# Optimization experiments

Measured on AMD Instinct MI355X. Metric: run time of the kernel, lower is better.

## Reference

```python
import jax, jax.numpy as jnp
import numpy as np

N = 200000
NNZ = 6400000
E = 500000
IN_P, IN_F, IN_N = 62, 37, 37
HID, LAT, DEC_HID = 256, 128, 64


def _p(key, shape, scale=0.05):
    return scale * jax.random.normal(key, shape, dtype=jnp.float32)


def setup_inputs() -> dict:
    key = jax.random.key(0)
    ks = jax.random.split(key, 32)
    inp = {
        'x_process': jax.random.normal(ks[0], (N, IN_P), dtype=jnp.float32),
        'x_file': jax.random.normal(ks[1], (N, IN_F), dtype=jnp.float32),
        'x_network': jax.random.normal(ks[2], (N, IN_N), dtype=jnp.float32),
        'adj_rows': jax.random.randint(ks[3], (NNZ,), 0, N, dtype=jnp.int32),
        'adj_cols': jax.random.randint(ks[4], (NNZ,), 0, N, dtype=jnp.int32),
        'adj_vals': jax.random.uniform(ks[5], (NNZ,), dtype=jnp.float32) / 32.0,
        'edge_src': jax.random.randint(ks[6], (E,), 0, N, dtype=jnp.int32),
        'edge_dst': jax.random.randint(ks[7], (E,), 0, N, dtype=jnp.int32),
        # per-view encoder params (weights stored [in, out])
        'Wp1': _p(ks[8], (IN_P, HID)), 'bp1': jnp.zeros((HID,), jnp.float32),
        'Wp2': _p(ks[9], (HID, LAT)), 'bp2': jnp.zeros((LAT,), jnp.float32),
        'Wf1': _p(ks[10], (IN_F, HID)), 'bf1': jnp.zeros((HID,), jnp.float32),
        'Wf2': _p(ks[11], (HID, LAT)), 'bf2': jnp.zeros((LAT,), jnp.float32),
        'Wn1': _p(ks[12], (IN_N, HID)), 'bn1': jnp.zeros((HID,), jnp.float32),
        'Wn2': _p(ks[13], (HID, LAT)), 'bn2': jnp.zeros((LAT,), jnp.float32),
        # gates
        'Wgp': _p(ks[14], (LAT, 1)), 'bgp': jnp.zeros((1,), jnp.float32),
        'Wgf': _p(ks[15], (LAT, 1)), 'bgf': jnp.zeros((1,), jnp.float32),
        'Wgn': _p(ks[16], (LAT, 1)), 'bgn': jnp.zeros((1,), jnp.float32),
        # mlp edge decoder
        'Wd1': _p(ks[17], (4 * LAT, DEC_HID)), 'bd1': jnp.zeros((DEC_HID,), jnp.float32),
        'Wd2': _p(ks[18], (DEC_HID, 1)), 'bd2': jnp.zeros((1,), jnp.float32),
    }
    return inp


def _spmm(rows, cols, vals, x):
    # sparse (COO) adjacency @ dense x : gather cols, scale, scatter-add into rows
    return jax.ops.segment_sum(vals[:, None] * x[cols], rows, num_segments=N)


def _encode_view(x, rows, cols, vals, W1, b1, W2, b2):
    h = jax.nn.relu(_spmm(rows, cols, vals, x) @ W1 + b1)  # dropout=0 / eval mode
    return _spmm(rows, cols, vals, h) @ W2 + b2


def reference(x_process, x_file, x_network, adj_rows, adj_cols, adj_vals,
              edge_src, edge_dst,
              Wp1, bp1, Wp2, bp2, Wf1, bf1, Wf2, bf2, Wn1, bn1, Wn2, bn2,
              Wgp, bgp, Wgf, bgf, Wgn, bgn, Wd1, bd1, Wd2, bd2):
    zp = _encode_view(x_process, adj_rows, adj_cols, adj_vals, Wp1, bp1, Wp2, bp2)
    zf = _encode_view(x_file, adj_rows, adj_cols, adj_vals, Wf1, bf1, Wf2, bf2)
    zn = _encode_view(x_network, adj_rows, adj_cols, adj_vals, Wn1, bn1, Wn2, bn2)
    # multi-view softmax gating -> fused latent [N, LAT]
    scores = jnp.concatenate([zp @ Wgp + bgp, zf @ Wgf + bgf, zn @ Wgn + bgn], axis=1)
    alpha = jax.nn.softmax(scores, axis=1)
    z = alpha[:, 0:1] * zp + alpha[:, 1:2] * zf + alpha[:, 2:3] * zn
    # mlp edge decoder: gather src/dst, concat features, small MLP
    zs, zd = z[edge_src], z[edge_dst]
    feats = jnp.concatenate([zs, zd, zs * zd, jnp.abs(zs - zd)], axis=1)  # [E, 4*LAT]
    logits = jax.nn.relu(feats @ Wd1 + bd1) @ Wd2 + bd2
    return logits[:, 0]
```

## Files before the change

### kernel.cpp

```cpp
#include <hip/hip_runtime.h>
#include <math.h>

#define Nn 200000
#define NNZV 6400000
#define NE 500000
#define HID 256
#define LAT 128

typedef _Float16 h2 __attribute__((ext_vector_type(2)));
typedef _Float16 f16x4 __attribute__((ext_vector_type(4)));
typedef _Float16 f16x8 __attribute__((ext_vector_type(8)));
typedef float f32x4 __attribute__((ext_vector_type(4)));
typedef short s16x8 __attribute__((ext_vector_type(8)));
struct alignas(8) H4 { _Float16 h[4]; };

__device__ __forceinline__ float rdlanef(float v, int k){
  return __uint_as_float(__builtin_amdgcn_readlane(__float_as_uint(v), k));
}

__global__ __launch_bounds__(256) void k_zero(int* __restrict__ cnt){
  int i = blockIdx.x*256 + threadIdx.x;
  if(i < Nn) cnt[i] = 0;
}

__global__ __launch_bounds__(256) void k_count(const int* __restrict__ rows, int* __restrict__ cnt){
  int i = blockIdx.x*256 + threadIdx.x;
  if(i < NNZV) atomicAdd(&cnt[rows[i]], 1);
}

__global__ __launch_bounds__(512) void k_scan_block(const int* __restrict__ cnt, int* __restrict__ incl, int* __restrict__ bsum){
  __shared__ int s[512];
  int t = threadIdx.x;
  int i = blockIdx.x*512 + t;
  int v = (i < Nn) ? cnt[i] : 0;
  s[t] = v; __syncthreads();
  for(int off = 1; off < 512; off <<= 1){
    int x = (t >= off) ? s[t-off] : 0;
    __syncthreads();
    s[t] += x;
    __syncthreads();
  }
  if(i < Nn) incl[i] = s[t];
  if(t == 511) bsum[blockIdx.x] = s[t];
}

__global__ __launch_bounds__(512) void k_scan_bsum(int* __restrict__ bsum, int nb){
  __shared__ int s[512];
  int t = threadIdx.x;
  int v = (t < nb) ? bsum[t] : 0;
  s[t] = v; __syncthreads();
  for(int off = 1; off < 512; off <<= 1){
    int x = (t >= off) ? s[t-off] : 0;
    __syncthreads();
    s[t] += x;
    __syncthreads();
  }
  if(t < nb) bsum[t] = s[t] - v;
}

__global__ __launch_bounds__(256) void k_finish(const int* __restrict__ incl, const int* __restrict__ boff, int* __restrict__ row_ptr){
  int i = blockIdx.x*256 + threadIdx.x;
  if(i < Nn) row_ptr[i+1] = incl[i] + boff[i >> 9];
  if(i == 0) row_ptr[0] = 0;
}

__global__ __launch_bounds__(256) void k_initcur(const int* __restrict__ row_ptr, int* __restrict__ cur){
  int i = blockIdx.x*256 + threadIdx.x;
  if(i < Nn) cur[i] = row_ptr[i];
}

__global__ __launch_bounds__(256) void k_scatter(const int* __restrict__ rows, const int* __restrict__ cols,
    const float* __restrict__ vals, int* __restrict__ cur,
    int* __restrict__ cols_s, _Float16* __restrict__ vals_s){
  int i = blockIdx.x*256 + threadIdx.x;
  if(i >= NNZV) return;
  int r = rows[i];
  int j = atomicAdd(&cur[r], 1);
  cols_s[j] = cols[i];
  vals_s[j] = (_Float16)vals[i];
}

__global__ __launch_bounds__(256) void k_xpack(const float* __restrict__ xp, const float* __restrict__ xf,
    const float* __restrict__ xn, _Float16* __restrict__ xc0, _Float16* __restrict__ xtl){
  int idx = blockIdx.x*256 + threadIdx.x;
  int row = idx/18, c8 = idx - row*18;
  if(row >= Nn) return;
  H4 ha, hb;
  #pragma unroll
  for(int q = 0; q < 8; q++){
    int c = c8*8 + q;
    float x;
    if(c < 62)       x = xp[row*62 + c];
    else if(c < 99)  x = xf[row*37 + (c-62)];
    else if(c == 99) x = 0.f;
    else if(c < 137) x = xn[row*37 + (c-100)];
    else             x = 0.f;
    if(q < 4) ha.h[q] = (_Float16)x; else hb.h[q-4] = (_Float16)x;
  }
  if(c8 < 16){
    *(H4*)&xc0[(size_t)row*128 + c8*8]     = ha;
    *(H4*)&xc0[(size_t)row*128 + c8*8 + 4] = hb;
  } else {
    int t = (c8-16)*8;
    *(H4*)&xtl[(size_t)row*16 + t]     = ha;
    *(H4*)&xtl[(size_t)row*16 + t + 4] = hb;
  }
}

__global__ __launch_bounds__(256) void k_wpackF(
    const float* __restrict__ Wp1, const float* __restrict__ Wf1, const float* __restrict__ Wn1,
    const float* __restrict__ Wp2, const float* __restrict__ Wf2, const float* __restrict__ Wn2,
    _Float16* __restrict__ w1fp, _Float16* __restrict__ w1ff, _Float16* __restrict__ w1fn,
    _Float16* __restrict__ w2fp, _Float16* __restrict__ w2ff, _Float16* __restrict__ w2fn){
  int i = blockIdx.x*256 + threadIdx.x;
  if(i >= 18432) return;
  int v = i / 6144, rem = i - v*6144;
  const float* W1 = (v==0)?Wp1:((v==1)?Wf1:Wn1);
  const float* W2 = (v==0)?Wp2:((v==1)?Wf2:Wn2);
  _Float16* d1 = (v==0)?w1fp:((v==1)?w1ff:w1fn);
  _Float16* d2 = (v==0)?w2fp:((v==1)?w2ff:w2fn);
  int Kv = (v==0)?62:37;
  f16x8 o;
  if(rem < 2048){
    int kt = rem >> 10, r2 = rem & 1023;
    int nt = r2 >> 6, l = r2 & 63;
    int krow = kt*32 + (l>>4)*8, col = nt*16 + (l&15);
    #pragma unroll
    for(int j = 0; j < 8; j++){
      int k = krow + j;
      o[j] = (k < Kv) ? (_Float16)W1[k*256 + col] : (_Float16)0.f;
    }
    *(f16x8*)&d1[rem*8] = o;
  } else {
    int r = rem - 2048;
    int kt = r >> 9, nt = (r >> 6) & 7, l = r & 63;
    int krow = kt*32 + (l>>4)*8, col = nt*16 + (l&15);
    #pragma unroll
    for(int j = 0; j < 8; j++)
      o[j] = (_Float16)W2[(krow + j)*128 + col];
    *(f16x8*)&d2[r*8] = o;
  }
}

__global__ void k_wg2(const float* __restrict__ Wp2, const float* __restrict__ Wgp,
                      const float* __restrict__ Wf2, const float* __restrict__ Wgf,
                      const float* __restrict__ Wn2, const float* __restrict__ Wgn,
                      float* __restrict__ wg2){
  int k = threadIdx.x;
  float p = 0.f, f = 0.f, n = 0.f;
  for(int c = 0; c < 128; c++){
    p = fmaf(Wp2[k*128 + c], Wgp[c], p);
    f = fmaf(Wf2[k*128 + c], Wgf[c], f);
    n = fmaf(Wn2[k*128 + c], Wgn[c], n);
  }
  wg2[k] = p; wg2[256 + k] = f; wg2[512 + k] = n;
}

__global__ void k_const(const float* b2p, const float* Wgp, const float* bgp,
                        const float* b2f, const float* Wgf, const float* bgf,
                        const float* b2n, const float* Wgn, const float* bgn,
                        float* c3){
  int l = threadIdx.x;
  float p = 0.f, f = 0.f, n = 0.f;
  for(int j = l; j < LAT; j += 64){
    p += b2p[j]*Wgp[j];
    f += b2f[j]*Wgf[j];
    n += b2n[j]*Wgn[j];
  }
  #pragma unroll
  for(int off = 32; off >= 1; off >>= 1){
    p += __shfl_xor(p, off);
    f += __shfl_xor(f, off);
    n += __shfl_xor(n, off);
  }
  if(l == 0){ c3[0] = p + bgp[0]; c3[1] = f + bgf[0]; c3[2] = n + bgn[0]; }
}

__device__ __forceinline__ void encode_view(
    int tid, int row0, int voff, int Kv, int vidx,
    const _Float16 (*sT)[152], _Float16 (*sTv)[72], _Float16 (*hT)[264],
    const _Float16* __restrict__ w1frag, const float* __restrict__ b1,
    const _Float16* __restrict__ w2frag, const float* __restrict__ wg2v,
    _Float16* __restrict__ Y3, float* __restrict__ yg4f){
  int w = tid >> 6, l = tid & 63;
  int kg = l >> 4, er = l & 15;
  int mrow = (w & 1)*16 + er;

  {
    int row = tid >> 3, c0 = (tid & 7)*8;
    f16x8 vv;
    #pragma unroll
    for(int q = 0; q < 8; q++){
      int c = c0 + q;
      vv[q] = (c < Kv) ? sT[row][voff + c] : (_Float16)0.f;
    }
    *(f16x8*)&sTv[row][c0] = vv;
  }
  __syncthreads();

  {
    f16x8 a0 = *(const f16x8*)&sTv[mrow][kg*8];
    f16x8 a1 = *(const f16x8*)&sTv[mrow][32 + kg*8];
    int ntb = (w >> 1)*8;
    #pragma unroll
    for(int nt8 = 0; nt8 < 8; nt8++){
      int nt = ntb + nt8;
      f16x8 b0 = *(const f16x8*)&w1frag[(size_t)((0*16 + nt)*64 + l)*8];
      f16x8 b1v = *(const f16x8*)&w1frag[(size_t)((1*16 + nt)*64 + l)*8];
      f32x4 acc = {0.f, 0.f, 0.f, 0.f};
      acc = __builtin_amdgcn_mfma_f32_16x16x32_f16(a0, b0, acc, 0, 0, 0);
      acc = __builtin_amdgcn_mfma_f32_16x16x32_f16(a1, b1v, acc, 0, 0, 0);
      int col = nt*16 + er;
      float bb = b1[col];
      #pragma unroll
      for(int j = 0; j < 4; j++)
        hT[(w & 1)*16 + kg*4 + j][col] = (_Float16)fmaxf(acc[j] + bb, 0.f);
    }
  }
  __syncthreads();

  {
    int row = tid >> 3, cg = tid & 7;
    float p = 0.f;
    #pragma unroll 8
    for(int kk = 0; kk < 32; kk++)
      p = fmaf((float)hT[row][cg*32 + kk], wg2v[cg*32 + kk], p);
    p += __shfl_xor(p, 1);
    p += __shfl_xor(p, 2);
    p += __shfl_xor(p, 4);
    if((tid & 7) == 0) yg4f[(size_t)(row0 + row)*4 + vidx] = p;
  }

  {
    f16x8 af[8];
    #pragma unroll
    for(int kt = 0; kt < 8; kt++)
      af[kt] = *(const f16x8*)&hT[mrow][kt*32 + kg*8];
    __syncthreads();
    _Float16* yst = &hT[0][0];
    int ntb = (w >> 1)*4;
    #pragma unroll
    for(int nt4 = 0; nt4 < 4; nt4++){
      int nt = ntb + nt4;
      f32x4 acc = {0.f, 0.f, 0.f, 0.f};
      #pragma unroll
      for(int kt = 0; kt < 8; kt++){
        f16x8 bf = *(const f16x8*)&w2frag[(size_t)((kt*8 + nt)*64 + l)*8];
        acc = __builtin_amdgcn_mfma_f32_16x16x32_f16(af[kt], bf, acc, 0, 0, 0);
      }
      int col = nt*16 + er;
      #pragma unroll
      for(int j = 0; j < 4; j++)
        yst[((w & 1)*16 + kg*4 + j)*132 + col] = (_Float16)acc[j];
    }
    __syncthreads();
    int row = tid >> 3, c0 = (tid & 7)*16;
    f16x8 y0 = *(const f16x8*)&yst[row*132 + c0];
    f16x8 y1 = *(const f16x8*)&yst[row*132 + c0 + 8];
    _Float16* yo = &Y3[(size_t)(row0 + row)*384 + vidx*128 + c0];
    *(f16x8*)yo       = y0;
    *(f16x8*)(yo + 8) = y1;
  }
  __syncthreads();
}

__global__ __launch_bounds__(256, 5) void k_encfused(
    const int* __restrict__ row_ptr, const int* __restrict__ cols_s, const _Float16* __restrict__ vals_s,
    const _Float16* __restrict__ xc0, const _Float16* __restrict__ xtl,
    const _Float16* __restrict__ w1fp, const float* __restrict__ bp1, const _Float16* __restrict__ w2fp,
    const _Float16* __restrict__ w1ff, const float* __restrict__ bf1, const _Float16* __restrict__ w2ff,
    const _Float16* __restrict__ w1fn, const float* __restrict__ bn1, const _Float16* __restrict__ w2fn,
    const float* __restrict__ wg2,
    _Float16* __restrict__ Y3, float* __restrict__ yg4f){
  __shared__ _Float16 sT[32][152];
  __shared__ _Float16 sTv[32][72];
  __shared__ _Float16 hT[32][264];
  int tid = threadIdx.x;
  int lane = tid & 63, wid = tid >> 6;
  int hl = lane & 31;
  int half = lane >> 5;
  int base = lane & 32;
  int row0 = blockIdx.x * 32;
  bool hast = (hl < 4);
  const char* xc0b = (const char*)xc0;
  const char* xtlb = (const char*)xtl;

  for(int p = 0; p < 4; p++){
    int rr = wid*8 + p*2 + half;
    int r = row0 + rr;
    int start = row_ptr[r], end = row_ptr[r+1];
    int len = end - start;
    int lenO = __shfl(len, lane ^ 32);
    int lenmax = len > lenO ? len : lenO;
    float a0 = 0.f, a1 = 0.f, a2 = 0.f, a3 = 0.f;
    float t0 = 0.f, t1 = 0.f, t2 = 0.f, t3 = 0.f;
    for(int j0 = 0; j0 < lenmax; j0 += 32){
      int m = len - j0; if(m > 32) m = 32; if(m < 0) m = 0;
      int mO = lenO - j0; if(mO > 32) mO = 32; if(mO < 0) mO = 0;
      int mmax = m > mO ? m : mO;
      int mycol = 0; float myval = 0.f;
      if(hl < m){
        mycol = cols_s[start + j0 + hl];
        myval = (float)vals_s[start + j0 + hl];
      }
      int mpad = (mmax + 3) & ~3;
      for(int k = 0; k < mpad; k += 4){
        #pragma unroll
        for(int q = 0; q < 4; q++){
          int c = __shfl(mycol, base + k + q);
          float v = __shfl(myval, base + k + q);
          f16x4 xa = *(const f16x4*)(xc0b + (((unsigned)c) << 8) + hl*8);
          a0 = fmaf((float)xa[0], v, a0);
          a1 = fmaf((float)xa[1], v, a1);
          a2 = fmaf((float)xa[2], v, a2);
          a3 = fmaf((float)xa[3], v, a3);
          if(hast){
            f16x4 xb = *(const f16x4*)(xtlb + ((unsigned)c)*32u + hl*8);
            t0 = fmaf((float)xb[0], v, t0);
            t1 = fmaf((float)xb[1], v, t1);
            t2 = fmaf((float)xb[2], v, t2);
            t3 = fmaf((float)xb[3], v, t3);
          }
        }
      }
    }
    h2 s01; s01[0] = (_Float16)a0; s01[1] = (_Float16)a1;
    h2 s23; s23[0] = (_Float16)a2; s23[1] = (_Float16)a3;
    *(h2*)&sT[rr][4*hl]     = s01;
    *(h2*)&sT[rr][4*hl + 2] = s23;
    if(hast){
      h2 u01; u01[0] = (_Float16)t0; u01[1] = (_Float16)t1;
      h2 u23; u23[0] = (_Float16)t2; u23[1] = (_Float16)t3;
      *(h2*)&sT[rr][128 + 4*hl]     = u01;
      *(h2*)&sT[rr][128 + 4*hl + 2] = u23;
    }
  }
  __syncthreads();

  encode_view(tid, row0, 0,   62, 0, sT, sTv, hT, w1fp, bp1, w2fp, wg2,       Y3, yg4f);
  encode_view(tid, row0, 62,  37, 1, sT, sTv, hT, w1ff, bf1, w2ff, wg2 + 256, Y3, yg4f);
  encode_view(tid, row0, 100, 37, 2, sT, sTv, hT, w1fn, bn1, w2fn, wg2 + 512, Y3, yg4f);
}

__global__ __launch_bounds__(256, 8) void k_spmm2f(
    const int* __restrict__ row_ptr, const int* __restrict__ cols_s, const _Float16* __restrict__ vals_s,
    const _Float16* __restrict__ Y3,
    const float4* __restrict__ yg4, const float* __restrict__ c3,
    const float* __restrict__ b2p, const float* __restrict__ b2f, const float* __restrict__ b2n,
    _Float16* __restrict__ z){
  int tid = threadIdx.x;
  int lane = tid & 63;
  int r = blockIdx.x*4 + (tid >> 6);
  int start = row_ptr[r], end = row_ptr[r+1];
  unsigned lo = lane*4;
  float ap0=0.f, ap1=0.f, af0=0.f, af1=0.f, an0=0.f, an1=0.f;
  float scp=0.f, scf=0.f, scn=0.f;
  const char* Yb = (const char*)Y3;
  for(int j0 = start; j0 < end; j0 += 64){
    int m = end - j0; if(m > 64) m = 64;
    int mycol = 0; float myval = 0.f;
    if(lane < m){
      mycol = cols_s[j0 + lane];
      myval = (float)vals_s[j0 + lane];
      float4 g = yg4[mycol];
      scp = fmaf(myval, g.x, scp);
      scf = fmaf(myval, g.y, scf);
      scn = fmaf(myval, g.z, scn);
    }
    int mpad = (m + 3) & ~3;
    for(int k = 0; k < mpad; k += 4){
      #pragma unroll
      for(int q = 0; q < 4; q++){
        int c = __builtin_amdgcn_readlane(mycol, k + q);
        float v = rdlanef(myval, k + q);
        const char* p = Yb + ((unsigned)c)*768u + lo;
        h2 yp = *(const h2*)(p);
        h2 yf = *(const h2*)(p + 256);
        h2 yn = *(const h2*)(p + 512);
        ap0 = fmaf((float)yp[0], v, ap0); ap1 = fmaf((float)yp[1], v, ap1);
        af0 = fmaf((float)yf[0], v, af0); af1 = fmaf((float)yf[1], v, af1);
        an0 = fmaf((float)yn[0], v, an0); an1 = fmaf((float)yn[1], v, an1);
      }
    }
  }
  #pragma unroll
  for(int off = 32; off >= 1; off >>= 1){
    scp += __shfl_xor(scp, off);
    scf += __shfl_xor(scf, off);
    scn += __shfl_xor(scn, off);
  }
  float sp = scp + c3[0], sf = scf + c3[1], sn = scn + c3[2];
  float mx = fmaxf(sp, fmaxf(sf, sn));
  float ep = expf(sp - mx), ef = expf(sf - mx), en = expf(sn - mx);
  float inv = 1.f / (ep + ef + en);
  float A0 = ep*inv, A1 = ef*inv, A2 = en*inv;
  int o = lane*2;
  float2 bp = *(const float2*)&b2p[o];
  float2 bf = *(const float2*)&b2f[o];
  float2 bn = *(const float2*)&b2n[o];
  float z0 = A0*(ap0 + bp.x) + A1*(af0 + bf.x) + A2*(an0 + bn.x);
  float z1 = A0*(ap1 + bp.y) + A1*(af1 + bf.y) + A2*(an1 + bn.y);
  h2 uz; uz[0] = (_Float16)z0; uz[1] = (_Float16)z1;
  *(h2*)&z[(size_t)r*LAT + o] = uz;
}

#define DEC_TILES (NE/16)
__global__ __launch_bounds__(256) void k_dec(
    const _Float16* __restrict__ z, const int* __restrict__ esrc, const int* __restrict__ edst,
    const float* __restrict__ Wd1, const float* __restrict__ bd1,
    const float* __restrict__ Wd2, const float* __restrict__ bd2, float* __restrict__ out){
  __shared__ float part[4][16][68];
  int tid = threadIdx.x;
  int w  = tid >> 6;
  int l  = tid & 63;
  int erow = l & 15;
  int kg   = l >> 4;

  f16x8 bfr[4][4];
  #pragma unroll
  for(int kt = 0; kt < 4; kt++){
    #pragma unroll
    for(int nt = 0; nt < 4; nt++){
      f16x8 bb;
      #pragma unroll
      for(int j = 0; j < 8; j++)
        bb[j] = (_Float16)Wd1[(w*128 + kt*32 + kg*8 + j)*64 + nt*16 + erow];
      bfr[kt][nt] = bb;
    }
  }

  int n0 = (tid & 15) * 4;
  int e2 = tid >> 4;
  float4 bb1 = *(const float4*)&bd1[n0];
  float4 w2v = *(const float4*)&Wd2[n0];
  float bias2 = bd2[0];

  for(int tile = blockIdx.x; tile < DEC_TILES; tile += gridDim.x){
    int e = tile*16 + erow;
    int si = esrc[e], di = edst[e];
    const f16x8* zs = (const f16x8*)&z[(size_t)si*LAT];
    const f16x8* zd = (const f16x8*)&z[(size_t)di*LAT];
    f16x8 afr[4];
    if(w == 0){
      #pragma unroll
      for(int kt = 0; kt < 4; kt++) afr[kt] = zs[kt*4 + kg];
    } else if(w == 1){
      #pragma unroll
      for(int kt = 0; kt < 4; kt++) afr[kt] = zd[kt*4 + kg];
    } else if(w == 2){
      #pragma unroll
      for(int kt = 0; kt < 4; kt++) afr[kt] = zs[kt*4 + kg] * zd[kt*4 + kg];
    } else {
      #pragma unroll
      for(int kt = 0; kt < 4; kt++){
        f16x8 d = zs[kt*4 + kg] - zd[kt*4 + kg];
        s16x8 m = __builtin_bit_cast(s16x8, d) & (short)0x7fff;
        afr[kt] = __builtin_bit_cast(f16x8, m);
      }
    }
    f32x4 zero = {0.f, 0.f, 0.f, 0.f};
    f32x4 acc[4] = {zero, zero, zero, zero};
    #pragma unroll
    for(int kt = 0; kt < 4; kt++){
      #pragma unroll
      for(int nt = 0; nt < 4; nt++)
        acc[nt] = __builtin_amdgcn_mfma_f32_16x16x32_f16(afr[kt], bfr[kt][nt], acc[nt], 0, 0, 0);
    }
    #pragma unroll
    for(int nt = 0; nt < 4; nt++){
      #pragma unroll
      for(int j = 0; j < 4; j++)
        part[w][kg*4 + j][nt*16 + erow] = acc[nt][j];
    }
    __syncthreads();
    float s0 = part[0][e2][n0+0] + part[1][e2][n0+0] + part[2][e2][n0+0] + part[3][e2][n0+0];
    float s1 = part[0][e2][n0+1] + part[1][e2][n0+1] + part[2][e2][n0+1] + part[3][e2][n0+1];
    float s2 = part[0][e2][n0+2] + part[1][e2][n0+2] + part[2][e2][n0+2] + part[3][e2][n0+2];
    float s3 = part[0][e2][n0+3] + part[1][e2][n0+3] + part[2][e2][n0+3] + part[3][e2][n0+3];
    float p = fmaxf(s0 + bb1.x, 0.f)*w2v.x + fmaxf(s1 + bb1.y, 0.f)*w2v.y
            + fmaxf(s2 + bb1.z, 0.f)*w2v.z + fmaxf(s3 + bb1.w, 0.f)*w2v.w;
    #pragma unroll
    for(int off = 1; off < 16; off <<= 1) p += __shfl_xor(p, off);
    if((tid & 15) == 0) out[tile*16 + e2] = p + bias2;
    __syncthreads();
  }
}

extern "C" void kernel_launch(void* const* d_in, const int* in_sizes, int n_in,
                              void* d_out, int out_size, void* d_ws, size_t ws_size,
                              hipStream_t stream) {
  const float* xp  = (const float*)d_in[0];
  const float* xf  = (const float*)d_in[1];
  const float* xn  = (const float*)d_in[2];
  const int* arows = (const int*)d_in[3];
  const int* acols = (const int*)d_in[4];
  const float* avals = (const float*)d_in[5];
  const int* esrc  = (const int*)d_in[6];
  const int* edst  = (const int*)d_in[7];
  const float* Wp1 = (const float*)d_in[8];  const float* bp1 = (const float*)d_in[9];
  const float* Wp2 = (const float*)d_in[10]; const float* bp2 = (const float*)d_in[11];
  const float* Wf1 = (const float*)d_in[12]; const float* bf1 = (const float*)d_in[13];
  const float* Wf2 = (const float*)d_in[14]; const float* bf2w = (const float*)d_in[15];
  const float* Wn1 = (const float*)d_in[16]; const float* bn1 = (const float*)d_in[17];
  const float* Wn2 = (const float*)d_in[18]; const float* bn2 = (const float*)d_in[19];
  const float* Wgp = (const float*)d_in[20]; const float* bgp = (const float*)d_in[21];
  const float* Wgf = (const float*)d_in[22]; const float* bgf = (const float*)d_in[23];
  const float* Wgn = (const float*)d_in[24]; const float* bgn = (const float*)d_in[25];
  const float* Wd1 = (const float*)d_in[26]; const float* bd1 = (const float*)d_in[27];
  const float* Wd2 = (const float*)d_in[28]; const float* bd2 = (const float*)d_in[29];
  float* out = (float*)d_out;
  (void)in_sizes; (void)n_in; (void)out_size; (void)ws_size;

  char* base = (char*)d_ws;
  size_t off = 0;
  auto alloc = [&](size_t nbytes) -> char* {
    off = (off + 255) & ~(size_t)255;
    char* p = base + off;
    off += nbytes;
    return p;
  };
  int*      row_ptr = (int*)     alloc((size_t)(Nn + 1) * 4);
  int*      cols_s  = (int*)     alloc((size_t)NNZV * 4);
  _Float16* vals_s  = (_Float16*)alloc((size_t)NNZV * 2);
  _Float16* xcat0   = (_Float16*)alloc((size_t)Nn * 128 * 2);
  _Float16* xtail   = (_Float16*)alloc((size_t)Nn * 16 * 2);
  _Float16* Y3      = (_Float16*)alloc((size_t)Nn * 384 * 2);
  float*    yg4     = (float*)   alloc((size_t)Nn * 4 * 4);
  float*    c3      = (float*)   alloc(256);
  float*    wg2     = (float*)   alloc(3 * 256 * 4);
  _Float16* w1fp = (_Float16*)alloc(16384*2);
  _Float16* w1ff = (_Float16*)alloc(16384*2);
  _Float16* w1fn = (_Float16*)alloc(16384*2);
  _Float16* w2fp = (_Float16*)alloc(32768*2);
  _Float16* w2ff = (_Float16*)alloc(32768*2);
  _Float16* w2fn = (_Float16*)alloc(32768*2);
  _Float16* z = xcat0;
  int* cur  = (int*)((char*)xcat0);
  int* incl = (int*)((char*)xcat0 + 1000000);
  int* bsum = (int*)((char*)xcat0 + 2000000);

  int NB = (Nn + 511) / 512;

  k_zero   <<<(Nn + 255)/256, 256, 0, stream>>>(cur);
  k_count  <<<(NNZV + 255)/256, 256, 0, stream>>>(arows, cur);
  k_scan_block<<<NB, 512, 0, stream>>>(cur, incl, bsum);
  k_scan_bsum<<<1, 512, 0, stream>>>(bsum, NB);
  k_finish <<<(Nn + 255)/256, 256, 0, stream>>>(incl, bsum, row_ptr);
  k_initcur<<<(Nn + 255)/256, 256, 0, stream>>>(row_ptr, cur);
  k_scatter<<<(NNZV + 255)/256, 256, 0, stream>>>(arows, acols, avals, cur, cols_s, vals_s);

  k_xpack<<<(Nn*18 + 255)/256, 256, 0, stream>>>(xp, xf, xn, xcat0, xtail);
  k_wpackF<<<72, 256, 0, stream>>>(Wp1, Wf1, Wn1, Wp2, Wf2, Wn2,
                                   w1fp, w1ff, w1fn, w2fp, w2ff, w2fn);
  k_wg2<<<1, 256, 0, stream>>>(Wp2, Wgp, Wf2, Wgf, Wn2, Wgn, wg2);
  k_const<<<1, 64, 0, stream>>>(bp2, Wgp, bgp, bf2w, Wgf, bgf, bn2, Wgn, bgn, c3);

  k_encfused<<<Nn/32, 256, 0, stream>>>(row_ptr, cols_s, vals_s, xcat0, xtail,
      w1fp, bp1, w2fp,  w1ff, bf1, w2ff,  w1fn, bn1, w2fn,  wg2,
      Y3, yg4);

  k_spmm2f<<<Nn/4, 256, 0, stream>>>(row_ptr, cols_s, vals_s, Y3,
      (const float4*)yg4, c3, bp2, bf2w, bn2, z);

  k_dec<<<2048, 256, 0, stream>>>(z, esrc, edst, Wd1, bd1, Wd2, bd2, out);
}
```

Baseline: 2.292 ms.

## Process two rows per wavefront in second SpMM and fuse cursor init into scan finish

The second SpMM kernel now gives each half-wavefront (32 lanes) its own row, and each lane loads 8-byte fp16 vectors per view instead of 4-byte ones. This doubles rows per block and widens the per-lane gathers to use more of each memory request. Column and value broadcast moves from readlane to cross-lane shuffles, and both halves loop to the longer row's length, which can waste work when the two rows differ in length. Separately, the cursor initialisation kernel is merged into the prefix-scan finish kernel, removing one launch and one pass over the row pointers.

Result: no change. 2.308 ms (+0.7%).

```diff
diff --git a/kernel.cpp b/kernel.cpp
--- a/kernel.cpp
+++ b/kernel.cpp
@@ -58,15 +58,15 @@
   if(t < nb) bsum[t] = s[t] - v;
 }
 
-__global__ __launch_bounds__(256) void k_finish(const int* __restrict__ incl, const int* __restrict__ boff, int* __restrict__ row_ptr){
+__global__ __launch_bounds__(256) void k_finish(const int* __restrict__ incl, const int* __restrict__ boff,
+                                                int* __restrict__ row_ptr, int* __restrict__ cur){
   int i = blockIdx.x*256 + threadIdx.x;
-  if(i < Nn) row_ptr[i+1] = incl[i] + boff[i >> 9];
-  if(i == 0) row_ptr[0] = 0;
-}
-
-__global__ __launch_bounds__(256) void k_initcur(const int* __restrict__ row_ptr, int* __restrict__ cur){
-  int i = blockIdx.x*256 + threadIdx.x;
-  if(i < Nn) cur[i] = row_ptr[i];
+  if(i < Nn){
+    int v = incl[i] + boff[i >> 9];
+    row_ptr[i+1] = v;
+    if(i < Nn-1) cur[i+1] = v;
+  }
+  if(i == 0){ row_ptr[0] = 0; cur[0] = 0; }
 }
 
 __global__ __launch_bounds__(256) void k_scatter(const int* __restrict__ rows, const int* __restrict__ cols,
@@ -350,41 +350,54 @@
     _Float16* __restrict__ z){
   int tid = threadIdx.x;
   int lane = tid & 63;
-  int r = blockIdx.x*4 + (tid >> 6);
+  int hl = lane & 31;
+  int half = lane >> 5;
+  int base = lane & 32;
+  int r = blockIdx.x*8 + (tid >> 6)*2 + half;
   int start = row_ptr[r], end = row_ptr[r+1];
-  unsigned lo = lane*4;
-  float ap0=0.f, ap1=0.f, af0=0.f, af1=0.f, an0=0.f, an1=0.f;
+  int len = end - start;
+  int lenO = __shfl(len, lane ^ 32);
+  int lenmax = len > lenO ? len : lenO;
+  unsigned lo = hl*8;
+  float ap0=0.f, ap1=0.f, ap2=0.f, ap3=0.f;
+  float af0=0.f, af1=0.f, af2=0.f, af3=0.f;
+  float an0=0.f, an1=0.f, an2=0.f, an3=0.f;
   float scp=0.f, scf=0.f, scn=0.f;
   const char* Yb = (const char*)Y3;
-  for(int j0 = start; j0 < end; j0 += 64){
-    int m = end - j0; if(m > 64) m = 64;
+  for(int j0 = 0; j0 < lenmax; j0 += 32){
+    int m = len - j0; if(m > 32) m = 32; if(m < 0) m = 0;
+    int mO = lenO - j0; if(mO > 32) mO = 32; if(mO < 0) mO = 0;
+    int mmax = m > mO ? m : mO;
     int mycol = 0; float myval = 0.f;
-    if(lane < m){
-      mycol = cols_s[j0 + lane];
-      myval = (float)vals_s[j0 + lane];
+    if(hl < m){
+      mycol = cols_s[start + j0 + hl];
+      myval = (float)vals_s[start + j0 + hl];
       float4 g = yg4[mycol];
       scp = fmaf(myval, g.x, scp);
       scf = fmaf(myval, g.y, scf);
       scn = fmaf(myval, g.z, scn);
     }
-    int mpad = (m + 3) & ~3;
+    int mpad = (mmax + 3) & ~3;
     for(int k = 0; k < mpad; k += 4){
       #pragma unroll
       for(int q = 0; q < 4; q++){
-        int c = __builtin_amdgcn_readlane(mycol, k + q);
-        float v = rdlanef(myval, k + q);
+        int c = __shfl(mycol, base + k + q);
+        float v = __shfl(myval, base + k + q);
         const char* p = Yb + ((unsigned)c)*768u + lo;
-        h2 yp = *(const h2*)(p);
-        h2 yf = *(const h2*)(p + 256);
-        h2 yn = *(const h2*)(p + 512);
+        f16x4 yp = *(const f16x4*)(p);
+        f16x4 yf = *(const f16x4*)(p + 256);
+        f16x4 yn = *(const f16x4*)(p + 512);
         ap0 = fmaf((float)yp[0], v, ap0); ap1 = fmaf((float)yp[1], v, ap1);
+        ap2 = fmaf((float)yp[2], v, ap2); ap3 = fmaf((float)yp[3], v, ap3);
         af0 = fmaf((float)yf[0], v, af0); af1 = fmaf((float)yf[1], v, af1);
+        af2 = fmaf((float)yf[2], v, af2); af3 = fmaf((float)yf[3], v, af3);
         an0 = fmaf((float)yn[0], v, an0); an1 = fmaf((float)yn[1], v, an1);
+        an2 = fmaf((float)yn[2], v, an2); an3 = fmaf((float)yn[3], v, an3);
       }
     }
   }
   #pragma unroll
-  for(int off = 32; off >= 1; off >>= 1){
+  for(int off = 16; off >= 1; off >>= 1){
     scp += __shfl_xor(scp, off);
     scf += __shfl_xor(scf, off);
     scn += __shfl_xor(scn, off);
@@ -394,14 +407,16 @@
   float ep = expf(sp - mx), ef = expf(sf - mx), en = expf(sn - mx);
   float inv = 1.f / (ep + ef + en);
   float A0 = ep*inv, A1 = ef*inv, A2 = en*inv;
-  int o = lane*2;
-  float2 bp = *(const float2*)&b2p[o];
-  float2 bf = *(const float2*)&b2f[o];
-  float2 bn = *(const float2*)&b2n[o];
-  float z0 = A0*(ap0 + bp.x) + A1*(af0 + bf.x) + A2*(an0 + bn.x);
-  float z1 = A0*(ap1 + bp.y) + A1*(af1 + bf.y) + A2*(an1 + bn.y);
-  h2 uz; uz[0] = (_Float16)z0; uz[1] = (_Float16)z1;
-  *(h2*)&z[(size_t)r*LAT + o] = uz;
+  int o = hl*4;
+  float4 bp = *(const float4*)&b2p[o];
+  float4 bf = *(const float4*)&b2f[o];
+  float4 bn = *(const float4*)&b2n[o];
+  H4 uz;
+  uz.h[0] = (_Float16)(A0*(ap0 + bp.x) + A1*(af0 + bf.x) + A2*(an0 + bn.x));
+  uz.h[1] = (_Float16)(A0*(ap1 + bp.y) + A1*(af1 + bf.y) + A2*(an1 + bn.y));
+  uz.h[2] = (_Float16)(A0*(ap2 + bp.z) + A1*(af2 + bf.z) + A2*(an2 + bn.z));
+  uz.h[3] = (_Float16)(A0*(ap3 + bp.w) + A1*(af3 + bf.w) + A2*(an3 + bn.w));
+  *(H4*)&z[(size_t)r*LAT + o] = uz;
 }
 
 #define DEC_TILES (NE/16)
@@ -545,8 +560,7 @@
   k_count  <<<(NNZV + 255)/256, 256, 0, stream>>>(arows, cur);
   k_scan_block<<<NB, 512, 0, stream>>>(cur, incl, bsum);
   k_scan_bsum<<<1, 512, 0, stream>>>(bsum, NB);
-  k_finish <<<(Nn + 255)/256, 256, 0, stream>>>(incl, bsum, row_ptr);
-  k_initcur<<<(Nn + 255)/256, 256, 0, stream>>>(row_ptr, cur);
+  k_finish <<<(Nn + 255)/256, 256, 0, stream>>>(incl, bsum, row_ptr, cur);
   k_scatter<<<(NNZV + 255)/256, 256, 0, stream>>>(arows, acols, avals, cur, cols_s, vals_s);
 
   k_xpack<<<(Nn*18 + 255)/256, 256, 0, stream>>>(xp, xf, xn, xcat0, xtail);
@@ -559,7 +573,7 @@
       w1fp, bp1, w2fp,  w1ff, bf1, w2ff,  w1fn, bn1, w2fn,  wg2,
       Y3, yg4);
 
-  k_spmm2f<<<Nn/4, 256, 0, stream>>>(row_ptr, cols_s, vals_s, Y3,
+  k_spmm2f<<<Nn/8, 256, 0, stream>>>(row_ptr, cols_s, vals_s, Y3,
       (const float4*)yg4, c3, bp2, bf2w, bn2, z);
 
   k_dec<<<2048, 256, 0, stream>>>(z, esrc, edst, Wd1, bd1, Wd2, bd2, out);
```
